# Optimization experiments

Measured on AMD Instinct MI355X. Metric: run time of the kernel, lower is better.

The kernel has to match this reference:

```python
import jax, jax.numpy as jnp
import numpy as np

N_NODES = 160000
N_EDGES = 2560000
N_GRAPHS = 1024
D = 32


def _gcn_layer(x, W, b, row, col, w):
    # PyG GCNConv with add_self_loops=True (loop weight 1) and symmetric norm.
    xw = x @ W                                   # [N, D]
    deg = jax.ops.segment_sum(w, col, num_segments=N_NODES) + 1.0  # self-loop
    dinv = jax.lax.rsqrt(deg)                    # deg >= 1 so finite
    norm = dinv[row] * w * dinv[col]             # [E]
    agg = jax.ops.segment_sum(norm[:, None] * xw[row], col, num_segments=N_NODES)
    agg = agg + xw * (1.0 / deg)[:, None]        # self-loop message: dinv[i]^2 = 1/deg[i]
    return agg + b


def setup_inputs() -> dict:
    key = jax.random.key(0)
    ks = jax.random.split(key, 20)
    s = 0.1
    inp = {
        "x": jax.random.normal(ks[0], (N_NODES, 1), jnp.float32),
        "edge_indices": jax.random.randint(ks[1], (2, N_EDGES), 0, N_NODES),
        "edge_weights": jax.random.uniform(ks[2], (N_EDGES,), jnp.float32),
        "batch": jnp.sort(jax.random.randint(ks[3], (N_NODES,), 0, N_GRAPHS)),
        # pre-MLP (2 layers)
        "W_pre0": s * jax.random.normal(ks[4], (1, D), jnp.float32),
        "b_pre0": jnp.zeros((D,), jnp.float32),
        "W_pre1": s * jax.random.normal(ks[5], (D, D), jnp.float32),
        "b_pre1": jnp.zeros((D,), jnp.float32),
        # 3 GCNConv layers
        "W_g0": s * jax.random.normal(ks[6], (D, D), jnp.float32),
        "b_g0": jnp.zeros((D,), jnp.float32),
        "W_g1": s * jax.random.normal(ks[7], (D, D), jnp.float32),
        "b_g1": jnp.zeros((D,), jnp.float32),
        "W_g2": s * jax.random.normal(ks[8], (D, D), jnp.float32),
        "b_g2": jnp.zeros((D,), jnp.float32),
        # post-MLP (2 layers, last -> 1 + sigmoid)
        "W_post0": s * jax.random.normal(ks[9], (D, D), jnp.float32),
        "b_post0": jnp.zeros((D,), jnp.float32),
        "W_post1": s * jax.random.normal(ks[10], (D, 1), jnp.float32),
        "b_post1": jnp.zeros((1,), jnp.float32),
    }
    return inp


def reference(x, edge_indices, edge_weights, batch,
              W_pre0, b_pre0, W_pre1, b_pre1,
              W_g0, b_g0, W_g1, b_g1, W_g2, b_g2,
              W_post0, b_post0, W_post1, b_post1):
    row, col = edge_indices[0], edge_indices[1]
    # pre-MLP: Linear + ReLU x2
    h = jax.nn.relu(x @ W_pre0 + b_pre0)
    h = jax.nn.relu(h @ W_pre1 + b_pre1)
    h = jax.nn.relu(_gcn_layer(h, W_g0, b_g0, row, col, edge_weights))
    h = jax.nn.relu(_gcn_layer(h, W_g1, b_g1, row, col, edge_weights))
    h = jax.nn.relu(_gcn_layer(h, W_g2, b_g2, row, col, edge_weights))
    # global mean pool over batch ids
    sums = jax.ops.segment_sum(h, batch, num_segments=N_GRAPHS)
    cnts = jax.ops.segment_sum(jnp.ones((N_NODES,), h.dtype), batch, num_segments=N_GRAPHS)
    g = sums / jnp.maximum(cnts, 1.0)[:, None]
    # post-MLP: Linear+ReLU (dropout inactive in eval), then Linear+Sigmoid
    g = jax.nn.relu(g @ W_post0 + b_post0)
    out = jax.nn.sigmoid(g @ W_post1 + b_post1)
    return out
```

## Files before the change

kernel.cpp:

```cpp
#include <hip/hip_runtime.h>
#include <math.h>

#define DIM 32
#define NB 625
#define CAP 5120

typedef float floatx2 __attribute__((ext_vector_type(2)));

__device__ __forceinline__ unsigned pack4_fp8(float a, float b, float c, float d) {
    unsigned v = 0;
    v = __builtin_amdgcn_cvt_pk_fp8_f32(a, b, v, false);
    v = __builtin_amdgcn_cvt_pk_fp8_f32(c, d, v, true);
    return v;
}

__global__ void setup_kernel(const int* __restrict__ batch, int* __restrict__ gptr,
                             int* __restrict__ bcur, int N, int G) {
    int n = blockIdx.x * blockDim.x + threadIdx.x;
    if (n < NB) bcur[n] = n * CAP;
    if (n >= N) return;
    int b = batch[n];
    int bp = (n == 0) ? -1 : batch[n - 1];
    for (int g = bp + 1; g <= b; g++) gptr[g] = n;
    if (n == N - 1) {
        for (int g = b + 1; g <= G; g++) gptr[g] = N;
    }
}

__global__ void passA_kernel(const int* __restrict__ row, const int* __restrict__ col,
                             const float* __restrict__ w, int* __restrict__ bcur,
                             unsigned long long* __restrict__ stage, int E) {
    __shared__ int hist[NB];
    __shared__ int lcur[NB];
    int base = blockIdx.x * 8192;
    int creg[8];
    for (int j = threadIdx.x; j < NB; j += 1024) hist[j] = 0;
    __syncthreads();
#pragma unroll
    for (int i = 0; i < 8; i++) {
        int e = base + i * 1024 + threadIdx.x;
        creg[i] = (e < E) ? col[e] : -1;
        if (e < E) atomicAdd(&hist[creg[i] >> 8], 1);
    }
    __syncthreads();
    for (int j = threadIdx.x; j < NB; j += 1024) {
        int h = hist[j];
        lcur[j] = h ? atomicAdd(&bcur[j], h) : 0;
    }
    __syncthreads();
#pragma unroll
    for (int i = 0; i < 8; i++) {
        int e = base + i * 1024 + threadIdx.x;
        if (e < E) {
            int c = creg[i];
            int b = c >> 8;
            int pos = atomicAdd(&lcur[b], 1);
            if (pos < (b + 1) * CAP) {
                unsigned long long rec = ((unsigned long long)(unsigned)row[e] << 40)
                                       | ((unsigned long long)(unsigned)(c & 255) << 32)
                                       | (unsigned long long)__float_as_uint(w[e]);
                stage[pos] = rec;
            }
        }
    }
}

__global__ void passB1_kernel(const unsigned long long* __restrict__ stage,
                              const int* __restrict__ bcur,
                              int* __restrict__ cnt, float* __restrict__ dinv) {
    __shared__ int icnt[256];
    __shared__ float fdeg[256];
    int b = blockIdx.x;
    icnt[threadIdx.x] = 0;
    fdeg[threadIdx.x] = 0.0f;
    __syncthreads();
    int s0 = b * CAP;
    int m = min(bcur[b] - s0, CAP);
    for (int i = threadIdx.x; i < m; i += 256) {
        unsigned long long rec = stage[s0 + i];
        int cj = (int)((rec >> 32) & 255);
        float wf = __uint_as_float((unsigned)rec);
        atomicAdd(&icnt[cj], 1);
        atomicAdd(&fdeg[cj], wf);
    }
    __syncthreads();
    int c = b * 256 + threadIdx.x;
    cnt[c] = icnt[threadIdx.x];
    dinv[c] = rsqrtf(fdeg[threadIdx.x] + 1.0f);
}

__global__ void scan_block_kernel(const int* __restrict__ cnt, int* __restrict__ ptr,
                                  int* __restrict__ bsum, int N) {
    __shared__ int s[256];
    int i = blockIdx.x * 256 + threadIdx.x;
    int v = (i < N) ? cnt[i] : 0;
    s[threadIdx.x] = v;
    __syncthreads();
#pragma unroll
    for (int off = 1; off < 256; off <<= 1) {
        int t = (threadIdx.x >= off) ? s[threadIdx.x - off] : 0;
        __syncthreads();
        s[threadIdx.x] += t;
        __syncthreads();
    }
    if (i < N) ptr[i] = s[threadIdx.x] - v;
    if (threadIdx.x == 255) bsum[blockIdx.x] = s[255];
}

__global__ void scan_fin_kernel(int* __restrict__ ptr, const int* __restrict__ bsum,
                                int N, int E) {
    __shared__ int red[256];
    int b = blockIdx.x;
    int t = threadIdx.x;
    int p = 0;
    for (int j = t; j < b; j += 256) p += bsum[j];
    red[t] = p;
    __syncthreads();
#pragma unroll
    for (int off = 128; off > 0; off >>= 1) {
        if (t < off) red[t] += red[t + off];
        __syncthreads();
    }
    int S = red[0];
    int i = b * 256 + t;
    if (i < N) ptr[i] += S;
    if (i == 0) ptr[N] = E;
}

__global__ void passB2_kernel(const unsigned long long* __restrict__ stage,
                              const int* __restrict__ bcur, const int* __restrict__ ptr,
                              const float* __restrict__ dinv,
                              unsigned* __restrict__ edat) {
    __shared__ int lcur[256];
    int b = blockIdx.x;
    lcur[threadIdx.x] = ptr[b * 256 + threadIdx.x];
    __syncthreads();
    int s0 = b * CAP;
    int m = min(bcur[b] - s0, CAP);
    for (int i = threadIdx.x; i < m; i += 256) {
        unsigned long long rec = stage[s0 + i];
        int r = (int)(rec >> 40);
        int cj = (int)((rec >> 32) & 255);
        float wf = __uint_as_float((unsigned)rec);
        float nm = dinv[r] * wf * dinv[b * 256 + cj];
        unsigned q = (unsigned)(nm * 16384.0f + 0.5f);
        q = min(q, 16383u);
        int pos = atomicAdd(&lcur[cj], 1);
        edat[pos] = ((unsigned)r << 14) | q;
    }
}

__global__ void pre_kernel(const float* __restrict__ x,
                           const float* __restrict__ W0, const float* __restrict__ b0,
                           const float* __restrict__ W1, const float* __restrict__ b1,
                           const float* __restrict__ Wg,
                           unsigned char* __restrict__ xw8, int N) {
    int n = blockIdx.x * blockDim.x + threadIdx.x;
    if (n >= N) return;
    float xv = x[n];
    float h0[DIM];
#pragma unroll
    for (int k = 0; k < DIM; k++) h0[k] = fmaxf(xv * W0[k] + b0[k], 0.0f);
    float h1[DIM];
#pragma unroll
    for (int d = 0; d < DIM; d++) h1[d] = b1[d];
#pragma unroll
    for (int k = 0; k < DIM; k++) {
        float hk = h0[k];
#pragma unroll
        for (int d = 0; d < DIM; d++) h1[d] += hk * W1[k * DIM + d];
    }
#pragma unroll
    for (int d = 0; d < DIM; d++) h1[d] = fmaxf(h1[d], 0.0f);
    float o[DIM];
#pragma unroll
    for (int d = 0; d < DIM; d++) o[d] = 0.0f;
#pragma unroll
    for (int k = 0; k < DIM; k++) {
        float hk = h1[k];
#pragma unroll
        for (int d = 0; d < DIM; d++) o[d] += hk * Wg[k * DIM + d];
    }
    unsigned u[8];
#pragma unroll
    for (int i = 0; i < 8; i++)
        u[i] = pack4_fp8(o[4 * i], o[4 * i + 1], o[4 * i + 2], o[4 * i + 3]);
    uint4* dst = (uint4*)(xw8 + (size_t)n * 32);
    dst[0] = make_uint4(u[0], u[1], u[2], u[3]);
    dst[1] = make_uint4(u[4], u[5], u[6], u[7]);
}

__global__ void mid_kernel(const float* __restrict__ agg, const float* __restrict__ Wg,
                           unsigned char* __restrict__ xw8, int N) {
    __shared__ float hs[64 * 33];
    __shared__ float wsm[32 * 32];
    int t = threadIdx.x;
    int base = blockIdx.x * 64;
    for (int j = t; j < 1024; j += 256) wsm[j] = Wg[j];
    const float4* src = (const float4*)(agg + (size_t)base * DIM);
#pragma unroll
    for (int m = 0; m < 2; m++) {
        int j4 = t + m * 256;
        float4 v = src[j4];
        int j = j4 * 4;
        float* hp = &hs[(j >> 5) * 33 + (j & 31)];
        hp[0] = fmaxf(v.x, 0.0f);
        hp[1] = fmaxf(v.y, 0.0f);
        hp[2] = fmaxf(v.z, 0.0f);
        hp[3] = fmaxf(v.w, 0.0f);
    }
    __syncthreads();
    int ln = t >> 2, sub = t & 3;
    const float* hrow = &hs[ln * 33];
    float o[8] = {0, 0, 0, 0, 0, 0, 0, 0};
#pragma unroll
    for (int k = 0; k < DIM; k++) {
        float hk = hrow[k];
        const float* wr = &wsm[k * DIM + sub * 8];
#pragma unroll
        for (int m = 0; m < 8; m++) o[m] += hk * wr[m];
    }
    unsigned u0 = pack4_fp8(o[0], o[1], o[2], o[3]);
    unsigned u1 = pack4_fp8(o[4], o[5], o[6], o[7]);
    *(uint2*)(xw8 + (size_t)(base + ln) * 32 + sub * 8) = make_uint2(u0, u1);
}

__global__ void gather_kernel(const unsigned char* __restrict__ xw8,
                              const unsigned* __restrict__ edat,
                              const int* __restrict__ ptr, const float* __restrict__ dinv,
                              const float* __restrict__ bg,
                              float* __restrict__ agg, int N) {
    int wv = (blockIdx.x * blockDim.x + threadIdx.x) >> 6;
    int n0 = wv * 4;
    if (n0 >= N) return;
    int lane = threadIdx.x & 63;
    int sg   = lane >> 4;
    int slot = (lane >> 2) & 3;
    int sub  = lane & 3;
    int n = n0 + sg;
    int e0 = ptr[n], e1 = ptr[n + 1];
    int terms = e1 - e0 + 1;
    float di = dinv[n];
    float acc[8] = {0, 0, 0, 0, 0, 0, 0, 0};
    for (int base = 0; base < terms; base += 4) {
        int idx = base + slot;
        int r; float nm;
        if (idx == 0) {
            r = n; nm = di * di;
        } else {
            int ee = e0 + idx - 1;
            ee = max(min(ee, e1 - 1), 0);
            unsigned rec = edat[ee];
            r = (int)(rec >> 14);
            nm = (float)(rec & 16383u) * (1.0f / 16384.0f);
        }
        if (idx >= terms) nm = 0.0f;
        const uint2* rp = (const uint2*)(xw8 + (size_t)r * 32 + sub * 8);
        uint2 u = *rp;
        floatx2 p0 = __builtin_amdgcn_cvt_pk_f32_fp8(u.x, false);
        floatx2 p1 = __builtin_amdgcn_cvt_pk_f32_fp8(u.x, true);
        floatx2 p2 = __builtin_amdgcn_cvt_pk_f32_fp8(u.y, false);
        floatx2 p3 = __builtin_amdgcn_cvt_pk_f32_fp8(u.y, true);
        acc[0] += nm * p0.x;
        acc[1] += nm * p0.y;
        acc[2] += nm * p1.x;
        acc[3] += nm * p1.y;
        acc[4] += nm * p2.x;
        acc[5] += nm * p2.y;
        acc[6] += nm * p3.x;
        acc[7] += nm * p3.y;
    }
#pragma unroll
    for (int s = 8; s >= 4; s >>= 1) {
#pragma unroll
        for (int i = 0; i < 8; i++) acc[i] += __shfl_xor(acc[i], s, 64);
    }
    if (slot == 0) {
        float4 v0 = make_float4(acc[0] + bg[sub * 8 + 0], acc[1] + bg[sub * 8 + 1],
                                acc[2] + bg[sub * 8 + 2], acc[3] + bg[sub * 8 + 3]);
        float4 v1 = make_float4(acc[4] + bg[sub * 8 + 4], acc[5] + bg[sub * 8 + 5],
                                acc[6] + bg[sub * 8 + 6], acc[7] + bg[sub * 8 + 7]);
        float4* dst = (float4*)(agg + (size_t)n * DIM + sub * 8);
        dst[0] = v0;
        dst[1] = v1;
    }
}

__global__ void pool_post_kernel(const float* __restrict__ agg, const int* __restrict__ gptr,
                                 const float* __restrict__ W0, const float* __restrict__ b0,
                                 const float* __restrict__ W1, const float* __restrict__ b1,
                                 float* __restrict__ out) {
    __shared__ float red[8][DIM];
    __shared__ float gv[DIM];
    __shared__ float pr[DIM];
    int g = blockIdx.x;
    int s0 = gptr[g], s1 = gptr[g + 1];
    int slot = threadIdx.x >> 5, d = threadIdx.x & 31;
    float acc = 0.0f;
    for (int n = s0 + slot; n < s1; n += 8)
        acc += fmaxf(agg[(size_t)n * DIM + d], 0.0f);
    red[slot][d] = acc;
    __syncthreads();
    if (threadIdx.x < DIM) {
        float t = 0.0f;
#pragma unroll
        for (int i = 0; i < 8; i++) t += red[i][threadIdx.x];
        float c = fmaxf((float)(s1 - s0), 1.0f);
        gv[threadIdx.x] = t / c;
    }
    __syncthreads();
    if (threadIdx.x < DIM) {
        int j = threadIdx.x;
        float p = b0[j];
#pragma unroll
        for (int k = 0; k < DIM; k++) p += gv[k] * W0[k * DIM + j];
        pr[j] = fmaxf(p, 0.0f) * W1[j];
    }
    __syncthreads();
    if (threadIdx.x == 0) {
        float a = b1[0];
#pragma unroll
        for (int j = 0; j < DIM; j++) a += pr[j];
        out[g] = 1.0f / (1.0f + expf(-a));
    }
}

extern "C" void kernel_launch(void* const* d_in, const int* in_sizes, int n_in,
                              void* d_out, int out_size, void* d_ws, size_t ws_size,
                              hipStream_t stream) {
    const float* x   = (const float*)d_in[0];
    const int*   ei  = (const int*)d_in[1];
    const float* ew  = (const float*)d_in[2];
    const int*   bat = (const int*)d_in[3];
    const float* Wpre0 = (const float*)d_in[4];
    const float* bpre0 = (const float*)d_in[5];
    const float* Wpre1 = (const float*)d_in[6];
    const float* bpre1 = (const float*)d_in[7];
    const float* Wg[3]  = {(const float*)d_in[8],  (const float*)d_in[10], (const float*)d_in[12]};
    const float* bg[3]  = {(const float*)d_in[9],  (const float*)d_in[11], (const float*)d_in[13]};
    const float* Wpost0 = (const float*)d_in[14];
    const float* bpost0 = (const float*)d_in[15];
    const float* Wpost1 = (const float*)d_in[16];
    const float* bpost1 = (const float*)d_in[17];
    float* out = (float*)d_out;

    const int N = in_sizes[0];
    const int E = in_sizes[2];
    const int G = out_size;
    const int nb = (N + 255) / 256;

    const int* row = ei;
    const int* col = ei + E;

    float* ws = (float*)d_ws;
    size_t nd = (size_t)N * DIM;
    float*          agg   = ws;
    unsigned char*  xw8   = (unsigned char*)(agg + nd);
    unsigned long long* stage = (unsigned long long*)ws;
    float*          dinv  = ws + nd + nd / 4;
    int*            cnt   = (int*)(dinv + N);
    int*            ptr   = cnt + N;
    int*            bsum  = ptr + (N + 2);
    int*            gptr  = bsum + 626;
    int*            bcur  = gptr + 1026;
    unsigned*       edat  = (unsigned*)(bcur + 626);

    const int B = 256;

    setup_kernel<<<(N + B - 1) / B, B, 0, stream>>>(bat, gptr, bcur, N, G);
    int nChunksA = (E + 8191) / 8192;
    passA_kernel<<<nChunksA, 1024, 0, stream>>>(row, col, ew, bcur, stage, E);
    passB1_kernel<<<NB, B, 0, stream>>>(stage, bcur, cnt, dinv);
    scan_block_kernel<<<nb, 256, 0, stream>>>(cnt, ptr, bsum, N);
    scan_fin_kernel<<<nb, 256, 0, stream>>>(ptr, bsum, N, E);
    passB2_kernel<<<NB, B, 0, stream>>>(stage, bcur, ptr, dinv, edat);

    pre_kernel<<<(N + B - 1) / B, B, 0, stream>>>(
        x, Wpre0, bpre0, Wpre1, bpre1, Wg[0], xw8, N);

    long long gThreads = (long long)(N / 4) * 64;
    int gBlocks = (int)((gThreads + B - 1) / B);
    int mBlocks = N / 64;

    gather_kernel<<<gBlocks, B, 0, stream>>>(xw8, edat, ptr, dinv, bg[0], agg, N);
    mid_kernel<<<mBlocks, B, 0, stream>>>(agg, Wg[1], xw8, N);
    gather_kernel<<<gBlocks, B, 0, stream>>>(xw8, edat, ptr, dinv, bg[1], agg, N);
    mid_kernel<<<mBlocks, B, 0, stream>>>(agg, Wg[2], xw8, N);
    gather_kernel<<<gBlocks, B, 0, stream>>>(xw8, edat, ptr, dinv, bg[2], agg, N);

    pool_post_kernel<<<G, 256, 0, stream>>>(agg, gptr, Wpost0, bpost0, Wpost1, bpost1, out);
}
```

Before: 350.7 us.

## Stage bucketed edge records in LDS and write them out coalesced in passA

```diff
diff --git a/kernel.cpp b/kernel.cpp
--- a/kernel.cpp
+++ b/kernel.cpp
@@ -4,6 +4,7 @@
 #define DIM 32
 #define NB 625
 #define CAP 5120
+#define CHUNK 8192
 
 typedef float floatx2 __attribute__((ext_vector_type(2)));
 
@@ -27,41 +28,72 @@
     }
 }
 
-__global__ void passA_kernel(const int* __restrict__ row, const int* __restrict__ col,
-                             const float* __restrict__ w, int* __restrict__ bcur,
-                             unsigned long long* __restrict__ stage, int E) {
+__global__ __launch_bounds__(1024) void passA_kernel(
+        const int* __restrict__ row, const int* __restrict__ col,
+        const float* __restrict__ w, int* __restrict__ bcur,
+        unsigned long long* __restrict__ stage, int E) {
+    __shared__ unsigned long long lrec[CHUNK];
     __shared__ int hist[NB];
-    __shared__ int lcur[NB];
-    int base = blockIdx.x * 8192;
+    __shared__ int excl[NB + 1];
+    __shared__ int gbase[NB];
+    __shared__ int sc[1024];
+    int t = threadIdx.x;
+    int base = blockIdx.x * CHUNK;
+    int cnt = min(CHUNK, E - base);
     int creg[8];
-    for (int j = threadIdx.x; j < NB; j += 1024) hist[j] = 0;
-    __syncthreads();
+
+    for (int j = t; j < NB; j += 1024) hist[j] = 0;
+    __syncthreads();
+
 #pragma unroll
     for (int i = 0; i < 8; i++) {
-        int e = base + i * 1024 + threadIdx.x;
+        int e = base + i * 1024 + t;
         creg[i] = (e < E) ? col[e] : -1;
-        if (e < E) atomicAdd(&hist[creg[i] >> 8], 1);
-    }
-    __syncthreads();
-    for (int j = threadIdx.x; j < NB; j += 1024) {
-        int h = hist[j];
-        lcur[j] = h ? atomicAdd(&bcur[j], h) : 0;
-    }
-    __syncthreads();
+        if (creg[i] >= 0) atomicAdd(&hist[creg[i] >> 8], 1);
+    }
+    __syncthreads();
+
+    int v = (t < NB) ? hist[t] : 0;
+    sc[t] = v;
+    __syncthreads();
+#pragma unroll
+    for (int off = 1; off < 1024; off <<= 1) {
+        int u = (t >= off) ? sc[t - off] : 0;
+        __syncthreads();
+        sc[t] += u;
+        __syncthreads();
+    }
+    if (t < NB) {
+        int ex = sc[t] - v;
+        excl[t] = ex;
+        hist[t] = ex;
+        gbase[t] = v ? atomicAdd(&bcur[t], v) : 0;
+    }
+    if (t == 0) excl[NB] = cnt;
+    __syncthreads();
+
 #pragma unroll
     for (int i = 0; i < 8; i++) {
-        int e = base + i * 1024 + threadIdx.x;
-        if (e < E) {
-            int c = creg[i];
-            int b = c >> 8;
-            int pos = atomicAdd(&lcur[b], 1);
-            if (pos < (b + 1) * CAP) {
-                unsigned long long rec = ((unsigned long long)(unsigned)row[e] << 40)
-                                       | ((unsigned long long)(unsigned)(c & 255) << 32)
-                                       | (unsigned long long)__float_as_uint(w[e]);
-                stage[pos] = rec;
-            }
+        int e = base + i * 1024 + t;
+        int c = creg[i];
+        if (c >= 0) {
+            unsigned long long rec = ((unsigned long long)(unsigned)row[e] << 40)
+                                   | ((unsigned long long)(unsigned)(c & 255) << 32)
+                                   | (unsigned long long)__float_as_uint(w[e]);
+            int pos = atomicAdd(&hist[c >> 8], 1);
+            lrec[pos] = rec;
         }
+    }
+    __syncthreads();
+
+    for (int i = t; i < cnt; i += 1024) {
+        int lo = 0, hi = NB;
+        while (hi - lo > 1) {
+            int mid = (lo + hi) >> 1;
+            if (excl[mid] <= i) lo = mid; else hi = mid;
+        }
+        int gpos = gbase[lo] + (i - excl[lo]);
+        if (gpos < (lo + 1) * CAP) stage[gpos] = lrec[i];
     }
 }
 
@@ -368,7 +400,7 @@
     const int B = 256;
 
     setup_kernel<<<(N + B - 1) / B, B, 0, stream>>>(bat, gptr, bcur, N, G);
-    int nChunksA = (E + 8191) / 8192;
+    int nChunksA = (E + CHUNK - 1) / CHUNK;
     passA_kernel<<<nChunksA, 1024, 0, stream>>>(row, col, ew, bcur, stage, E);
     passB1_kernel<<<NB, B, 0, stream>>>(stage, bcur, cnt, dinv);
     scan_block_kernel<<<nb, 256, 0, stream>>>(cnt, ptr, bsum, N);
```

Result: no change. 347.6 us (-0.9%).
